# Kernel optimization log

Measured on AMD Instinct MI355X. Metric: run time of the kernel, lower is better.

## Reference

```python
import jax, jax.numpy as jnp
import numpy as np

PATCH = 15  # box-filter kernel size (odd -> SAME padding == padding=PATCH//2, stride 1)


def _box_filter(x, k):
    """All-ones kxk conv2d, stride 1, zero pad k//2. x: (N,1,H,W).
    The ones kernel is separable: ones(k,k) = ones(k,1) @ ones(1,k)."""
    dn = ('NCHW', 'OIHW', 'NCHW')
    kh = jnp.ones((1, 1, k, 1), x.dtype)
    kw = jnp.ones((1, 1, 1, k), x.dtype)
    x = jax.lax.conv_general_dilated(x, kh, (1, 1), 'SAME', dimension_numbers=dn)
    x = jax.lax.conv_general_dilated(x, kw, (1, 1), 'SAME', dimension_numbers=dn)
    return x


def _rgb_to_yuv420(rgb):
    """rgb: (N,3,H,W) -> y:(N,H,W), u,v:(N,H/2,W/2) (2x2 avg-pooled chroma)."""
    r, g, b = rgb[:, 0], rgb[:, 1], rgb[:, 2]
    y = 0.299 * r + 0.587 * g + 0.114 * b
    u = -0.169 * r - 0.331 * g + 0.5 * b + 128.0
    v = 0.5 * r - 0.46 * g - 0.04 * b + 128.0
    n, h, w = u.shape
    u = u.reshape(n, h // 2, 2, w // 2, 2).mean(axis=(2, 4))
    v = v.reshape(n, h // 2, 2, w // 2, 2).mean(axis=(2, 4))
    return y, u, v


def _filtered_channels(img, k):
    y, u, v = _rgb_to_yuv420(img)
    return (_box_filter(y[:, None], k),
            _box_filter(u[:, None], k),
            _box_filter(v[:, None], k))


def setup_inputs() -> dict:
    key = jax.random.key(0)
    k1, k2 = jax.random.split(key)
    input_ = jax.random.uniform(k1, (16, 3, 512, 512), dtype=jnp.float32)
    target = jax.random.uniform(k2, (16, 3, 512, 512), dtype=jnp.float32)
    return {"input": input_, "target": target}


def reference(input, target):
    yi, ui, vi = _filtered_channels(input, PATCH)
    yt, ut, vt = _filtered_channels(target, PATCH)
    mse = lambda a, b: jnp.mean((a - b) ** 2)
    return mse(yi, yt) + mse(ui, ut) + mse(vi, vt)
```

## Files before the change

kernel.cpp:

```cpp
#include <hip/hip_runtime.h>

#define NIMG 16
#define H 512
#define W 512
#define HALF 7

#define RT 64
#define CT 256
#define YROWS 78
#define YCOLS 272
#define YSTR 276
#define CROWS 46
#define CCOLS 142
#define CSTR 152

static __device__ __forceinline__ unsigned short f2bf(float f) {
    unsigned u = __float_as_uint(f);
    u += 0x7FFFu + ((u >> 16) & 1u);
    return (unsigned short)(u >> 16);
}
static __device__ __forceinline__ float bf2f(unsigned short h) {
    return __uint_as_float(((unsigned)h) << 16);
}
static __device__ __forceinline__ float bflo(unsigned v) {
    return __uint_as_float(v << 16);
}
static __device__ __forceinline__ float bfhi(unsigned v) {
    return __uint_as_float(v & 0xFFFF0000u);
}

__global__ __launch_bounds__(512) void fused_loss_kernel(
        const float* __restrict__ in, const float* __restrict__ tgt,
        float invY, float invC, float* __restrict__ partials) {
    __shared__ float sY[YROWS * YSTR];
    __shared__ unsigned short sU[CROWS * CSTR];
    __shared__ unsigned short sV[CROWS * CSTR];
    __shared__ float part[8];

    const int tid = threadIdx.x;
    const int b = blockIdx.x;
    const int n  = b >> 4;
    const int rt = (b >> 1) & 7;
    const int ct = b & 1;
    const int r0 = rt << 6;
    const int c0 = ct << 8;

    const size_t plane = (size_t)H * W;
    const float* pi = in  + (size_t)n * 3 * plane;
    const float* pt = tgt + (size_t)n * 3 * plane;

#pragma unroll 2
    for (int i = tid; i < CROWS * 144; i += 512) {
        const int pr = i / 144;
        const int pc = i - pr * 144;
        const int yy = r0 - 14 + 2 * pr;
        const int xx = c0 - 14 + 2 * pc;

        float dr00=0.f,dr01=0.f,dr10=0.f,dr11=0.f;
        float dg00=0.f,dg01=0.f,dg10=0.f,dg11=0.f;
        float db00=0.f,db01=0.f,db10=0.f,db11=0.f;

        if ((unsigned)yy < H && (unsigned)xx < W && pc < CCOLS) {
            const int off = yy * W + xx;
            const float2 ir0 = *(const float2*)(pi + off);
            const float2 ir1 = *(const float2*)(pi + off + W);
            const float2 ig0 = *(const float2*)(pi + plane + off);
            const float2 ig1 = *(const float2*)(pi + plane + off + W);
            const float2 ib0 = *(const float2*)(pi + 2 * plane + off);
            const float2 ib1 = *(const float2*)(pi + 2 * plane + off + W);
            const float2 tr0 = *(const float2*)(pt + off);
            const float2 tr1 = *(const float2*)(pt + off + W);
            const float2 tg0 = *(const float2*)(pt + plane + off);
            const float2 tg1 = *(const float2*)(pt + plane + off + W);
            const float2 tb0 = *(const float2*)(pt + 2 * plane + off);
            const float2 tb1 = *(const float2*)(pt + 2 * plane + off + W);
            dr00 = ir0.x - tr0.x; dr01 = ir0.y - tr0.y;
            dr10 = ir1.x - tr1.x; dr11 = ir1.y - tr1.y;
            dg00 = ig0.x - tg0.x; dg01 = ig0.y - tg0.y;
            dg10 = ig1.x - tg1.x; dg11 = ig1.y - tg1.y;
            db00 = ib0.x - tb0.x; db01 = ib0.y - tb0.y;
            db10 = ib1.x - tb1.x; db11 = ib1.y - tb1.y;
        }

        const float y00 = 0.299f * dr00 + 0.587f * dg00 + 0.114f * db00;
        const float y01 = 0.299f * dr01 + 0.587f * dg01 + 0.114f * db01;
        const float y10 = 0.299f * dr10 + 0.587f * dg10 + 0.114f * db10;
        const float y11 = 0.299f * dr11 + 0.587f * dg11 + 0.114f * db11;

        const int ly0 = 2 * pr - 7;
        const int lx0 = 2 * pc - 6;
        if ((unsigned)lx0 < YCOLS) {
            if ((unsigned)ly0 < YROWS)
                *(float2*)&sY[ly0 * YSTR + lx0] = make_float2(y00, y01);
            if ((unsigned)(ly0 + 1) < YROWS)
                *(float2*)&sY[(ly0 + 1) * YSTR + lx0] = make_float2(y10, y11);
        }

        const float sr = dr00 + dr01 + dr10 + dr11;
        const float sg = dg00 + dg01 + dg10 + dg11;
        const float sb = db00 + db01 + db10 + db11;
        sU[pr * CSTR + pc] = f2bf((-0.169f * sr - 0.331f * sg + 0.5f  * sb) * 0.25f);
        sV[pr * CSTR + pc] = f2bf(( 0.5f   * sr - 0.46f  * sg - 0.04f * sb) * 0.25f);
    }
    __syncthreads();

    for (int t = tid; t < YCOLS + 2 * CCOLS; t += 512) {
        if (t < YCOLS) {
            const int j = t;
            float s = 0.f;
#pragma unroll
            for (int r = 0; r < 14; ++r) s += sY[r * YSTR + j];
#pragma unroll
            for (int y = 0; y < RT; ++y) {
                s += sY[(y + 14) * YSTR + j];
                const float o = s;
                s -= sY[y * YSTR + j];
                sY[y * YSTR + j] = o;
            }
        } else {
            const int jj = t - YCOLS;
            unsigned short* sp = (jj < CCOLS) ? sU : sV;
            const int j = (jj < CCOLS) ? jj : jj - CCOLS;
            float s = 0.f;
#pragma unroll
            for (int r = 0; r < 14; ++r) s += bf2f(sp[r * CSTR + j]);
#pragma unroll
            for (int y = 0; y < RT / 2; ++y) {
                s += bf2f(sp[(y + 14) * CSTR + j]);
                const float o = s;
                s -= bf2f(sp[y * CSTR + j]);
                sp[y * CSTR + j] = f2bf(o);
            }
        }
    }
    __syncthreads();

    float accY = 0.f, accC = 0.f;
    const int wv = tid >> 6, lane = tid & 63;

    {
        float wn[48];
        const int base = lane * YSTR + (wv << 5);
#pragma unroll
        for (int j = 0; j < 12; ++j)
            *(float4*)&wn[4 * j] = *(const float4*)&sY[base + 4 * j];
        float s = 0.f;
#pragma unroll
        for (int j = 1; j <= 14; ++j) s += wn[j];
#pragma unroll
        for (int k = 0; k < 32; ++k) {
            s += wn[15 + k];
            accY += s * s;
            s -= wn[1 + k];
        }
    }

    {
        const int pl = lane >> 5, y = lane & 31;
        const unsigned short* sp = pl ? sV : sU;
        const int base = y * CSTR + (wv << 4);
        float wn[32];
#pragma unroll
        for (int j = 0; j < 4; ++j) {
            const uint4 v = *(const uint4*)&sp[base + 8 * j];
            wn[8 * j + 0] = bflo(v.x); wn[8 * j + 1] = bfhi(v.x);
            wn[8 * j + 2] = bflo(v.y); wn[8 * j + 3] = bfhi(v.y);
            wn[8 * j + 4] = bflo(v.z); wn[8 * j + 5] = bfhi(v.z);
            wn[8 * j + 6] = bflo(v.w); wn[8 * j + 7] = bfhi(v.w);
        }
        float s = 0.f;
#pragma unroll
        for (int j = 0; j < 14; ++j) s += wn[j];
#pragma unroll
        for (int k = 0; k < 16; ++k) {
            s += wn[14 + k];
            accC += s * s;
            s -= wn[k];
        }
    }

    float v = accY * invY + accC * invC;
    for (int o = 32; o > 0; o >>= 1) v += __shfl_down(v, o, 64);
    if (lane == 0) part[wv] = v;
    __syncthreads();
    if (tid == 0) {
        float s = 0.f;
#pragma unroll
        for (int j = 0; j < 8; ++j) s += part[j];
        partials[b] = s;
    }
}

__global__ void final_reduce_kernel(const float* __restrict__ partials, int n,
                                    float* __restrict__ out) {
    float s = 0.f;
    for (int i = threadIdx.x; i < n; i += 256) s += partials[i];
    for (int o = 32; o > 0; o >>= 1) s += __shfl_down(s, o, 64);
    __shared__ float part[4];
    const int lane = threadIdx.x & 63, wid = threadIdx.x >> 6;
    if (lane == 0) part[wid] = s;
    __syncthreads();
    if (threadIdx.x == 0)
        *out = part[0] + part[1] + part[2] + part[3];
}

extern "C" void kernel_launch(void* const* d_in, const int* in_sizes, int n_in,
                              void* d_out, int out_size, void* d_ws, size_t ws_size,
                              hipStream_t stream) {
    const float* input  = (const float*)d_in[0];
    const float* target = (const float*)d_in[1];
    float* out = (float*)d_out;
    float* partials = (float*)d_ws;

    const float invY = 1.0f / (float)((size_t)NIMG * H * W);
    const float invC = 1.0f / (float)((size_t)NIMG * (H/2) * (W/2));

    fused_loss_kernel<<<NIMG * 8 * 2, 512, 0, stream>>>(input, target, invY, invC, partials);
    final_reduce_kernel<<<1, 256, 0, stream>>>(partials, NIMG * 8 * 2, out);
}
```

Before: 125.4 us.

## Halve column tile width, use float4 loads and packed bf16 chroma stores

Narrows the column tile from 256 to 128, doubling the grid to 512 blocks so more CUs have work and LDS per block shrinks, which allows higher occupancy (launch bounds now request 4 blocks). The load stage switches from float2 to float4 global loads, with each thread handling two chroma pixels and writing packed bf16 pairs. Halo overhead per tile grows because the 14-pixel halo is amortized over fewer output columns, so total global reads rise.

```diff
diff --git a/kernel.cpp b/kernel.cpp
--- a/kernel.cpp
+++ b/kernel.cpp
@@ -6,13 +6,13 @@
 #define HALF 7
 
 #define RT 64
-#define CT 256
+#define CT 128
 #define YROWS 78
-#define YCOLS 272
-#define YSTR 276
+#define YCOLS 144
+#define YSTR 148
 #define CROWS 46
-#define CCOLS 142
-#define CSTR 152
+#define CSTR 88
+#define NPAIR (CROWS * 40)
 
 static __device__ __forceinline__ unsigned short f2bf(float f) {
     unsigned u = __float_as_uint(f);
@@ -28,8 +28,11 @@
 static __device__ __forceinline__ float bfhi(unsigned v) {
     return __uint_as_float(v & 0xFFFF0000u);
 }
-
-__global__ __launch_bounds__(512) void fused_loss_kernel(
+static __device__ __forceinline__ unsigned pack2bf(float lo, float hi) {
+    return (unsigned)f2bf(lo) | ((unsigned)f2bf(hi) << 16);
+}
+
+__global__ __launch_bounds__(512, 4) void fused_loss_kernel(
         const float* __restrict__ in, const float* __restrict__ tgt,
         float invY, float invC, float* __restrict__ partials) {
     __shared__ float sY[YROWS * YSTR];
@@ -39,74 +42,80 @@
 
     const int tid = threadIdx.x;
     const int b = blockIdx.x;
-    const int n  = b >> 4;
-    const int rt = (b >> 1) & 7;
-    const int ct = b & 1;
+    const int n  = b >> 5;
+    const int rt = (b >> 2) & 7;
+    const int ct = b & 3;
     const int r0 = rt << 6;
-    const int c0 = ct << 8;
+    const int c0 = ct << 7;
 
     const size_t plane = (size_t)H * W;
     const float* pi = in  + (size_t)n * 3 * plane;
     const float* pt = tgt + (size_t)n * 3 * plane;
 
 #pragma unroll 2
-    for (int i = tid; i < CROWS * 144; i += 512) {
-        const int pr = i / 144;
-        const int pc = i - pr * 144;
+    for (int i = tid; i < NPAIR; i += 512) {
+        const int pr = i / 40;
+        const int q  = i - pr * 40;
         const int yy = r0 - 14 + 2 * pr;
-        const int xx = c0 - 14 + 2 * pc;
-
-        float dr00=0.f,dr01=0.f,dr10=0.f,dr11=0.f;
-        float dg00=0.f,dg01=0.f,dg10=0.f,dg11=0.f;
-        float db00=0.f,db01=0.f,db10=0.f,db11=0.f;
-
-        if ((unsigned)yy < H && (unsigned)xx < W && pc < CCOLS) {
-            const int off = yy * W + xx;
-            const float2 ir0 = *(const float2*)(pi + off);
-            const float2 ir1 = *(const float2*)(pi + off + W);
-            const float2 ig0 = *(const float2*)(pi + plane + off);
-            const float2 ig1 = *(const float2*)(pi + plane + off + W);
-            const float2 ib0 = *(const float2*)(pi + 2 * plane + off);
-            const float2 ib1 = *(const float2*)(pi + 2 * plane + off + W);
-            const float2 tr0 = *(const float2*)(pt + off);
-            const float2 tr1 = *(const float2*)(pt + off + W);
-            const float2 tg0 = *(const float2*)(pt + plane + off);
-            const float2 tg1 = *(const float2*)(pt + plane + off + W);
-            const float2 tb0 = *(const float2*)(pt + 2 * plane + off);
-            const float2 tb1 = *(const float2*)(pt + 2 * plane + off + W);
-            dr00 = ir0.x - tr0.x; dr01 = ir0.y - tr0.y;
-            dr10 = ir1.x - tr1.x; dr11 = ir1.y - tr1.y;
-            dg00 = ig0.x - tg0.x; dg01 = ig0.y - tg0.y;
-            dg10 = ig1.x - tg1.x; dg11 = ig1.y - tg1.y;
-            db00 = ib0.x - tb0.x; db01 = ib0.y - tb0.y;
-            db10 = ib1.x - tb1.x; db11 = ib1.y - tb1.y;
-        }
-
-        const float y00 = 0.299f * dr00 + 0.587f * dg00 + 0.114f * db00;
-        const float y01 = 0.299f * dr01 + 0.587f * dg01 + 0.114f * db01;
-        const float y10 = 0.299f * dr10 + 0.587f * dg10 + 0.114f * db10;
-        const float y11 = 0.299f * dr11 + 0.587f * dg11 + 0.114f * db11;
+        const int xx = c0 - 16 + 4 * q;
+
+        float4 dr0 = make_float4(0.f, 0.f, 0.f, 0.f), dr1 = dr0;
+        float4 dg0 = dr0, dg1 = dr0, db0 = dr0, db1 = dr0;
+
+        if ((unsigned)yy < H && (unsigned)xx < W) {
+            const size_t off = (size_t)yy * W + xx;
+            float4 a, t;
+            a = *(const float4*)(pi + off);              t = *(const float4*)(pt + off);
+            dr0 = make_float4(a.x - t.x, a.y - t.y, a.z - t.z, a.w - t.w);
+            a = *(const float4*)(pi + off + W);          t = *(const float4*)(pt + off + W);
+            dr1 = make_float4(a.x - t.x, a.y - t.y, a.z - t.z, a.w - t.w);
+            a = *(const float4*)(pi + plane + off);      t = *(const float4*)(pt + plane + off);
+            dg0 = make_float4(a.x - t.x, a.y - t.y, a.z - t.z, a.w - t.w);
+            a = *(const float4*)(pi + plane + off + W);  t = *(const float4*)(pt + plane + off + W);
+            dg1 = make_float4(a.x - t.x, a.y - t.y, a.z - t.z, a.w - t.w);
+            a = *(const float4*)(pi + 2*plane + off);    t = *(const float4*)(pt + 2*plane + off);
+            db0 = make_float4(a.x - t.x, a.y - t.y, a.z - t.z, a.w - t.w);
+            a = *(const float4*)(pi + 2*plane + off + W);t = *(const float4*)(pt + 2*plane + off + W);
+            db1 = make_float4(a.x - t.x, a.y - t.y, a.z - t.z, a.w - t.w);
+        }
+
+        float4 y0, y1;
+        y0.x = 0.299f*dr0.x + 0.587f*dg0.x + 0.114f*db0.x;
+        y0.y = 0.299f*dr0.y + 0.587f*dg0.y + 0.114f*db0.y;
+        y0.z = 0.299f*dr0.z + 0.587f*dg0.z + 0.114f*db0.z;
+        y0.w = 0.299f*dr0.w + 0.587f*dg0.w + 0.114f*db0.w;
+        y1.x = 0.299f*dr1.x + 0.587f*dg1.x + 0.114f*db1.x;
+        y1.y = 0.299f*dr1.y + 0.587f*dg1.y + 0.114f*db1.y;
+        y1.z = 0.299f*dr1.z + 0.587f*dg1.z + 0.114f*db1.z;
+        y1.w = 0.299f*dr1.w + 0.587f*dg1.w + 0.114f*db1.w;
 
         const int ly0 = 2 * pr - 7;
-        const int lx0 = 2 * pc - 6;
-        if ((unsigned)lx0 < YCOLS) {
+        const int lx  = 4 * q - 8;
+        if ((unsigned)lx < YCOLS) {
             if ((unsigned)ly0 < YROWS)
-                *(float2*)&sY[ly0 * YSTR + lx0] = make_float2(y00, y01);
+                *(float4*)&sY[ly0 * YSTR + lx] = y0;
             if ((unsigned)(ly0 + 1) < YROWS)
-                *(float2*)&sY[(ly0 + 1) * YSTR + lx0] = make_float2(y10, y11);
-        }
-
-        const float sr = dr00 + dr01 + dr10 + dr11;
-        const float sg = dg00 + dg01 + dg10 + dg11;
-        const float sb = db00 + db01 + db10 + db11;
-        sU[pr * CSTR + pc] = f2bf((-0.169f * sr - 0.331f * sg + 0.5f  * sb) * 0.25f);
-        sV[pr * CSTR + pc] = f2bf(( 0.5f   * sr - 0.46f  * sg - 0.04f * sb) * 0.25f);
-    }
-    __syncthreads();
-
-    for (int t = tid; t < YCOLS + 2 * CCOLS; t += 512) {
-        if (t < YCOLS) {
-            const int j = t;
+                *(float4*)&sY[(ly0 + 1) * YSTR + lx] = y1;
+        }
+
+        const float srA = dr0.x + dr0.y + dr1.x + dr1.y;
+        const float sgA = dg0.x + dg0.y + dg1.x + dg1.y;
+        const float sbA = db0.x + db0.y + db1.x + db1.y;
+        const float srB = dr0.z + dr0.w + dr1.z + dr1.w;
+        const float sgB = dg0.z + dg0.w + dg1.z + dg1.w;
+        const float sbB = db0.z + db0.w + db1.z + db1.w;
+        const float uA = (-0.169f*srA - 0.331f*sgA + 0.5f *sbA) * 0.25f;
+        const float vA = ( 0.5f  *srA - 0.46f *sgA - 0.04f*sbA) * 0.25f;
+        const float uB = (-0.169f*srB - 0.331f*sgB + 0.5f *sbB) * 0.25f;
+        const float vB = ( 0.5f  *srB - 0.46f *sgB - 0.04f*sbB) * 0.25f;
+        *(unsigned*)&sU[pr * CSTR + 2 * q] = pack2bf(uA, uB);
+        *(unsigned*)&sV[pr * CSTR + 2 * q] = pack2bf(vA, vB);
+    }
+    __syncthreads();
+
+    if (tid < 304) {
+        if (tid < YCOLS) {
+            const int j = tid;
             float s = 0.f;
 #pragma unroll
             for (int r = 0; r < 14; ++r) s += sY[r * YSTR + j];
@@ -118,9 +127,9 @@
                 sY[y * YSTR + j] = o;
             }
         } else {
-            const int jj = t - YCOLS;
-            unsigned short* sp = (jj < CCOLS) ? sU : sV;
-            const int j = (jj < CCOLS) ? jj : jj - CCOLS;
+            const int jj = tid - YCOLS;
+            unsigned short* sp = (jj < 80) ? sU : sV;
+            const int j = (jj < 80) ? jj : jj - 80;
             float s = 0.f;
 #pragma unroll
             for (int r = 0; r < 14; ++r) s += bf2f(sp[r * CSTR + j]);
@@ -139,16 +148,16 @@
     const int wv = tid >> 6, lane = tid & 63;
 
     {
-        float wn[48];
-        const int base = lane * YSTR + (wv << 5);
-#pragma unroll
-        for (int j = 0; j < 12; ++j)
+        float wn[32];
+        const int base = lane * YSTR + (wv << 4);
+#pragma unroll
+        for (int j = 0; j < 8; ++j)
             *(float4*)&wn[4 * j] = *(const float4*)&sY[base + 4 * j];
         float s = 0.f;
 #pragma unroll
         for (int j = 1; j <= 14; ++j) s += wn[j];
 #pragma unroll
-        for (int k = 0; k < 32; ++k) {
+        for (int k = 0; k < 16; ++k) {
             s += wn[15 + k];
             accY += s * s;
             s -= wn[1 + k];
@@ -158,10 +167,10 @@
     {
         const int pl = lane >> 5, y = lane & 31;
         const unsigned short* sp = pl ? sV : sU;
-        const int base = y * CSTR + (wv << 4);
-        float wn[32];
-#pragma unroll
-        for (int j = 0; j < 4; ++j) {
+        const int base = y * CSTR + (wv << 3);
+        float wn[24];
+#pragma unroll
+        for (int j = 0; j < 3; ++j) {
             const uint4 v = *(const uint4*)&sp[base + 8 * j];
             wn[8 * j + 0] = bflo(v.x); wn[8 * j + 1] = bfhi(v.x);
             wn[8 * j + 2] = bflo(v.y); wn[8 * j + 3] = bfhi(v.y);
@@ -170,12 +179,12 @@
         }
         float s = 0.f;
 #pragma unroll
-        for (int j = 0; j < 14; ++j) s += wn[j];
-#pragma unroll
-        for (int k = 0; k < 16; ++k) {
-            s += wn[14 + k];
+        for (int j = 1; j <= 14; ++j) s += wn[j];
+#pragma unroll
+        for (int k = 0; k < 8; ++k) {
+            s += wn[15 + k];
             accC += s * s;
-            s -= wn[k];
+            s -= wn[1 + k];
         }
     }
 
@@ -215,6 +224,6 @@
     const float invY = 1.0f / (float)((size_t)NIMG * H * W);
     const float invC = 1.0f / (float)((size_t)NIMG * (H/2) * (W/2));
 
-    fused_loss_kernel<<<NIMG * 8 * 2, 512, 0, stream>>>(input, target, invY, invC, partials);
-    final_reduce_kernel<<<1, 256, 0, stream>>>(partials, NIMG * 8 * 2, out);
-}
+    fused_loss_kernel<<<NIMG * 8 * 4, 512, 0, stream>>>(input, target, invY, invC, partials);
+    final_reduce_kernel<<<1, 256, 0, stream>>>(partials, NIMG * 8 * 4, out);
+}
```

Result: no change. 127.8 us (+1.9%).
